# Performance work log

Measured on AMD Instinct MI355X. Metric: run time of the kernel, lower is better.

Reference implementation:

```python
import jax, jax.numpy as jnp
import numpy as np

N_NODES = 100000

def setup_inputs() -> dict:
    key = jax.random.key(0)
    k1, k2, k3, k4, k5, k6 = jax.random.split(key, 6)
    n_edges = 3200000
    edge_rows = jnp.sort(jax.random.randint(k1, (n_edges,), 0, N_NODES))
    edge_cols = jax.random.randint(k2, (n_edges,), 0, N_NODES)
    edge_vals = jax.random.uniform(k3, (n_edges,), dtype=jnp.float32)
    h = jax.random.normal(k4, (N_NODES, 128), dtype=jnp.float32)
    W = jax.random.normal(k5, (128, 128), dtype=jnp.float32) * (1.0 / np.sqrt(128))
    b = jax.random.normal(k6, (128,), dtype=jnp.float32) * 0.01
    return {"edge_rows": edge_rows, "edge_cols": edge_cols, "edge_vals": edge_vals,
            "h": h, "W": W, "b": b}

def reference(edge_rows, edge_cols, edge_vals, h, W, b):
    # SpMM: out[i] = sum over edges e with row[e]==i of vals[e] * h[col[e]]
    msgs = edge_vals[:, None] * h[edge_cols]            # [E, d]
    agg = jax.ops.segment_sum(msgs, edge_rows, num_segments=N_NODES)  # [N, d]
    # Linear + activation (nn.Linear: x @ W.T + b)
    out = agg @ W.T + b
    return jax.nn.relu(out)
```

## Files before the change

kernel.cpp:

```cpp
#include <hip/hip_runtime.h>

#define N_NODES 100000
#define D 128

typedef unsigned short ushort_t;
typedef unsigned char uchar_t;
typedef __attribute__((ext_vector_type(8))) short short8;
typedef __attribute__((ext_vector_type(4))) float f32x4;

__device__ __forceinline__ unsigned f2bf(float x) {
    unsigned u = __float_as_uint(x);
    return (u + 0x7fffu + ((u >> 16) & 1u)) >> 16;
}

__global__ __launch_bounds__(64)
void build_wfrag_kernel(const float* __restrict__ W,
                        ushort_t* __restrict__ Wfrag) {
    const int t  = blockIdx.x;
    const int jt = t >> 2, kt = t & 3;
    const int l  = threadIdx.x;
    const float* src = W + (size_t)(jt * 16 + (l & 15)) * D + kt * 32 + (l >> 4) * 8;
    const float4 p0 = *reinterpret_cast<const float4*>(src);
    const float4 p1 = *reinterpret_cast<const float4*>(src + 4);
    uint4 o;
    o.x = f2bf(p0.x) | (f2bf(p0.y) << 16);
    o.y = f2bf(p0.z) | (f2bf(p0.w) << 16);
    o.z = f2bf(p1.x) | (f2bf(p1.y) << 16);
    o.w = f2bf(p1.z) | (f2bf(p1.w) << 16);
    *reinterpret_cast<uint4*>(Wfrag + ((size_t)t * 64 + l) * 8) = o;
}

__global__ __launch_bounds__(256)
void gemm_Gq_kernel(const float* __restrict__ h,
                    const ushort_t* __restrict__ Wfrag,
                    uchar_t* __restrict__ Gq,
                    float* __restrict__ scales) {
    const int wave = threadIdx.x >> 6;
    const int l    = threadIdx.x & 63;
    const int tile = blockIdx.x * 4 + wave;
    if (tile >= N_NODES / 16) return;
    const int n0   = tile * 16;
    const int lrow = l & 15;
    const int lk   = l >> 4;

    union { short8 v; ushort_t u[8]; } bfrag[4];
    const float* hp = h + (size_t)(n0 + lrow) * D + lk * 8;
#pragma unroll
    for (int kt = 0; kt < 4; ++kt) {
        const float4 q0 = *reinterpret_cast<const float4*>(hp + kt * 32);
        const float4 q1 = *reinterpret_cast<const float4*>(hp + kt * 32 + 4);
        bfrag[kt].u[0] = (ushort_t)f2bf(q0.x);
        bfrag[kt].u[1] = (ushort_t)f2bf(q0.y);
        bfrag[kt].u[2] = (ushort_t)f2bf(q0.z);
        bfrag[kt].u[3] = (ushort_t)f2bf(q0.w);
        bfrag[kt].u[4] = (ushort_t)f2bf(q1.x);
        bfrag[kt].u[5] = (ushort_t)f2bf(q1.y);
        bfrag[kt].u[6] = (ushort_t)f2bf(q1.z);
        bfrag[kt].u[7] = (ushort_t)f2bf(q1.w);
    }

    const uint4* wf = reinterpret_cast<const uint4*>(Wfrag) + l;
    f32x4 acc[8];
#pragma unroll
    for (int jt = 0; jt < 8; ++jt) {
        acc[jt] = (f32x4){0.f, 0.f, 0.f, 0.f};
#pragma unroll
        for (int kt = 0; kt < 4; ++kt) {
            union { uint4 q; short8 v; } af;
            af.q = wf[(jt * 4 + kt) * 64];
            acc[jt] = __builtin_amdgcn_mfma_f32_16x16x32_bf16(
                af.v, bfrag[kt].v, acc[jt], 0, 0, 0);
        }
    }

    float amax = 0.f;
#pragma unroll
    for (int jt = 0; jt < 8; ++jt) {
#pragma unroll
        for (int r = 0; r < 4; ++r) amax = fmaxf(amax, fabsf(acc[jt][r]));
    }
    amax = fmaxf(amax, __shfl_xor(amax, 16));
    amax = fmaxf(amax, __shfl_xor(amax, 32));
    const float s   = amax > 0.f ? amax * (1.f / 127.f) : 1.f;
    const float inv = amax > 0.f ? 127.f / amax : 0.f;

#pragma unroll
    for (int jt = 0; jt < 8; ++jt) {
        const unsigned q0 = (unsigned)((int)rintf(acc[jt][0] * inv) + 128);
        const unsigned q1 = (unsigned)((int)rintf(acc[jt][1] * inv) + 128);
        const unsigned q2 = (unsigned)((int)rintf(acc[jt][2] * inv) + 128);
        const unsigned q3 = (unsigned)((int)rintf(acc[jt][3] * inv) + 128);
        const unsigned pk = q0 | (q1 << 8) | (q2 << 16) | (q3 << 24);
        *reinterpret_cast<unsigned*>(
            Gq + (size_t)(n0 + lrow) * D + jt * 16 + lk * 4) = pk;
    }
    if (l < 16) scales[n0 + l] = s;
}

__global__ __launch_bounds__(256)
void prep_kernel(const int* __restrict__ rows,
                 const int* __restrict__ cols,
                 const float* __restrict__ vals,
                 const float* __restrict__ scales,
                 int* __restrict__ row_ptr,
                 float* __restrict__ vals2, int n_edges) {
    const int e = blockIdx.x * 256 + threadIdx.x;
    if (e >= n_edges) return;

    vals2[e] = vals[e] * scales[cols[e]];

    const int r0 = rows[e];
    if (e == 0) {
        for (int r = 0; r <= r0; ++r) row_ptr[r] = 0;
    }
    if (e + 1 < n_edges) {
        const int r1 = rows[e + 1];
        for (int r = r0 + 1; r <= r1; ++r) row_ptr[r] = e + 1;
    } else {
        for (int r = r0 + 1; r <= N_NODES; ++r) row_ptr[r] = n_edges;
    }
}

__device__ __forceinline__ void accq(float* a, float& vsum, float vs, uint2 g) {
    a[0] += vs * (float)(g.x & 0xffu);
    a[1] += vs * (float)((g.x >> 8) & 0xffu);
    a[2] += vs * (float)((g.x >> 16) & 0xffu);
    a[3] += vs * (float)(g.x >> 24);
    a[4] += vs * (float)(g.y & 0xffu);
    a[5] += vs * (float)((g.y >> 8) & 0xffu);
    a[6] += vs * (float)((g.y >> 16) & 0xffu);
    a[7] += vs * (float)(g.y >> 24);
    vsum += vs;
}

__global__ __launch_bounds__(256)
void gconv_gather_q_kernel(const int* __restrict__ cols,
                           const float* __restrict__ vals2,
                           const uchar_t* __restrict__ Gq,
                           const float* __restrict__ bias,
                           const int* __restrict__ row_ptr,
                           float* __restrict__ out) {
    const int tid  = blockIdx.x * 256 + threadIdx.x;
    const int node = tid >> 4;
    const int il   = tid & 15;
    const unsigned il8 = (unsigned)il * 8u;

    int e = row_ptr[node];
    const int end = row_ptr[node + 1];

    float a[8];
#pragma unroll
    for (int j = 0; j < 8; ++j) a[j] = 0.f;
    float vsum = 0.f;

    for (; e + 7 < end; e += 8) {
        int   c[8];
        float v[8];
        uint2 g[8];
#pragma unroll
        for (int i = 0; i < 8; ++i) c[i] = __builtin_nontemporal_load(cols + e + i);
#pragma unroll
        for (int i = 0; i < 8; ++i) v[i] = __builtin_nontemporal_load(vals2 + e + i);
#pragma unroll
        for (int i = 0; i < 8; ++i)
            g[i] = *reinterpret_cast<const uint2*>(Gq + (((unsigned)c[i] << 7) + il8));
#pragma unroll
        for (int i = 0; i < 8; ++i) accq(a, vsum, v[i], g[i]);
    }
    for (; e < end; ++e) {
        const int   c = __builtin_nontemporal_load(cols + e);
        const float v = __builtin_nontemporal_load(vals2 + e);
        const uint2 g = *reinterpret_cast<const uint2*>(Gq + (((unsigned)c << 7) + il8));
        accq(a, vsum, v, g);
    }

    const float4 b0 = *reinterpret_cast<const float4*>(bias + il8);
    const float4 b1 = *reinterpret_cast<const float4*>(bias + il8 + 4);
    const float corr = 128.f * vsum;
    f32x4 r0, r1;
    r0[0] = a[0] - corr + b0.x; r0[1] = a[1] - corr + b0.y;
    r0[2] = a[2] - corr + b0.z; r0[3] = a[3] - corr + b0.w;
    r1[0] = a[4] - corr + b1.x; r1[1] = a[5] - corr + b1.y;
    r1[2] = a[6] - corr + b1.z; r1[3] = a[7] - corr + b1.w;
#pragma unroll
    for (int i = 0; i < 4; ++i) {
        r0[i] = r0[i] > 0.f ? r0[i] : 0.f;
        r1[i] = r1[i] > 0.f ? r1[i] : 0.f;
    }
    float* op = out + (size_t)node * D + il8;
    __builtin_nontemporal_store(r0, reinterpret_cast<f32x4*>(op));
    __builtin_nontemporal_store(r1, reinterpret_cast<f32x4*>(op + 4));
}

extern "C" void kernel_launch(void* const* d_in, const int* in_sizes, int n_in,
                              void* d_out, int out_size, void* d_ws,
                              size_t ws_size, hipStream_t stream) {
    const int*   edge_rows = (const int*)d_in[0];
    const int*   edge_cols = (const int*)d_in[1];
    const float* edge_vals = (const float*)d_in[2];
    const float* h         = (const float*)d_in[3];
    const float* W         = (const float*)d_in[4];
    const float* b         = (const float*)d_in[5];
    float*       out       = (float*)d_out;

    const int n_edges = in_sizes[0];

    const size_t OFF_RP = 64 * 1024;
    const size_t OFF_SC = OFF_RP + 512 * 1024;
    const size_t OFF_GQ = OFF_SC + 512 * 1024;
    const size_t OFF_V2 = OFF_GQ + (size_t)N_NODES * D;

    ushort_t* Wfrag   = (ushort_t*)d_ws;
    int*      row_ptr = (int*)((char*)d_ws + OFF_RP);
    float*    scales  = (float*)((char*)d_ws + OFF_SC);
    uchar_t*  Gq      = (uchar_t*)((char*)d_ws + OFF_GQ);
    float*    vals2   = (float*)((char*)d_ws + OFF_V2);

    build_wfrag_kernel<<<32, 64, 0, stream>>>(W, Wfrag);

    const int n_tiles     = N_NODES / 16;
    const int gemm_blocks = (n_tiles + 3) / 4;
    gemm_Gq_kernel<<<gemm_blocks, 256, 0, stream>>>(h, Wfrag, Gq, scales);

    prep_kernel<<<(n_edges + 255) / 256, 256, 0, stream>>>(
        edge_rows, edge_cols, edge_vals, scales, row_ptr, vals2, n_edges);

    const int gather_blocks = N_NODES * 16 / 256;
    gconv_gather_q_kernel<<<gather_blocks, 256, 0, stream>>>(
        edge_cols, vals2, Gq, b, row_ptr, out);
}
```

Before: 145.1 us.

## Interleave col/val pairs and gather 16 bytes per lane with 8 lanes per node

The prep kernel now writes column index and scaled value as interleaved int2 pairs, so the gather loads one 8-byte pair per edge instead of two separate streams. The gather kernel drops from 16 to 8 lanes per node, with each lane loading 16 bytes of the quantized row and keeping 16 accumulators. This halves the redundant edge-metadata loads per node and widens each gather load. In exchange it doubles register pressure per thread, halves the thread count, and replaces the nontemporal output stores with plain stores.

New measurement: 129.3 us. 10.9% less time.

```diff
diff --git a/kernel.cpp b/kernel.cpp
--- a/kernel.cpp
+++ b/kernel.cpp
@@ -103,11 +103,12 @@
                  const float* __restrict__ vals,
                  const float* __restrict__ scales,
                  int* __restrict__ row_ptr,
-                 float* __restrict__ vals2, int n_edges) {
+                 int2* __restrict__ pairs, int n_edges) {
     const int e = blockIdx.x * 256 + threadIdx.x;
     if (e >= n_edges) return;
 
-    vals2[e] = vals[e] * scales[cols[e]];
+    const int c = cols[e];
+    pairs[e] = make_int2(c, __float_as_int(vals[e] * scales[c]));
 
     const int r0 = rows[e];
     if (e == 0) {
@@ -121,75 +122,72 @@
     }
 }
 
-__device__ __forceinline__ void accq(float* a, float& vsum, float vs, uint2 g) {
-    a[0] += vs * (float)(g.x & 0xffu);
-    a[1] += vs * (float)((g.x >> 8) & 0xffu);
-    a[2] += vs * (float)((g.x >> 16) & 0xffu);
-    a[3] += vs * (float)(g.x >> 24);
-    a[4] += vs * (float)(g.y & 0xffu);
-    a[5] += vs * (float)((g.y >> 8) & 0xffu);
-    a[6] += vs * (float)((g.y >> 16) & 0xffu);
-    a[7] += vs * (float)(g.y >> 24);
+__device__ __forceinline__ void accq16(float* a, float& vsum, float vs,
+                                       uint4 g) {
+    const unsigned w[4] = {g.x, g.y, g.z, g.w};
+#pragma unroll
+    for (int k = 0; k < 4; ++k) {
+        a[4 * k + 0] += vs * (float)(w[k] & 0xffu);
+        a[4 * k + 1] += vs * (float)((w[k] >> 8) & 0xffu);
+        a[4 * k + 2] += vs * (float)((w[k] >> 16) & 0xffu);
+        a[4 * k + 3] += vs * (float)(w[k] >> 24);
+    }
     vsum += vs;
 }
 
 __global__ __launch_bounds__(256)
-void gconv_gather_q_kernel(const int* __restrict__ cols,
-                           const float* __restrict__ vals2,
-                           const uchar_t* __restrict__ Gq,
-                           const float* __restrict__ bias,
-                           const int* __restrict__ row_ptr,
-                           float* __restrict__ out) {
+void gconv_gather_g8_kernel(const int2* __restrict__ pairs,
+                            const uchar_t* __restrict__ Gq,
+                            const float* __restrict__ bias,
+                            const int* __restrict__ row_ptr,
+                            float* __restrict__ out) {
     const int tid  = blockIdx.x * 256 + threadIdx.x;
-    const int node = tid >> 4;
-    const int il   = tid & 15;
-    const unsigned il8 = (unsigned)il * 8u;
+    const int node = tid >> 3;
+    const int il   = tid & 7;
+    const unsigned il16 = (unsigned)il * 16u;
 
     int e = row_ptr[node];
     const int end = row_ptr[node + 1];
 
-    float a[8];
-#pragma unroll
-    for (int j = 0; j < 8; ++j) a[j] = 0.f;
+    float a[16];
+#pragma unroll
+    for (int j = 0; j < 16; ++j) a[j] = 0.f;
     float vsum = 0.f;
 
     for (; e + 7 < end; e += 8) {
-        int   c[8];
-        float v[8];
-        uint2 g[8];
-#pragma unroll
-        for (int i = 0; i < 8; ++i) c[i] = __builtin_nontemporal_load(cols + e + i);
-#pragma unroll
-        for (int i = 0; i < 8; ++i) v[i] = __builtin_nontemporal_load(vals2 + e + i);
+        int2  p[8];
+        uint4 g[8];
+#pragma unroll
+        for (int i = 0; i < 8; ++i) p[i] = pairs[e + i];
 #pragma unroll
         for (int i = 0; i < 8; ++i)
-            g[i] = *reinterpret_cast<const uint2*>(Gq + (((unsigned)c[i] << 7) + il8));
-#pragma unroll
-        for (int i = 0; i < 8; ++i) accq(a, vsum, v[i], g[i]);
+            g[i] = *reinterpret_cast<const uint4*>(
+                Gq + (((unsigned)p[i].x << 7) + il16));
+#pragma unroll
+        for (int i = 0; i < 8; ++i)
+            accq16(a, vsum, __int_as_float(p[i].y), g[i]);
     }
     for (; e < end; ++e) {
-        const int   c = __builtin_nontemporal_load(cols + e);
-        const float v = __builtin_nontemporal_load(vals2 + e);
-        const uint2 g = *reinterpret_cast<const uint2*>(Gq + (((unsigned)c << 7) + il8));
-        accq(a, vsum, v, g);
-    }
-
-    const float4 b0 = *reinterpret_cast<const float4*>(bias + il8);
-    const float4 b1 = *reinterpret_cast<const float4*>(bias + il8 + 4);
+        const int2 p = pairs[e];
+        const uint4 g = *reinterpret_cast<const uint4*>(
+            Gq + (((unsigned)p.x << 7) + il16));
+        accq16(a, vsum, __int_as_float(p.y), g);
+    }
+
     const float corr = 128.f * vsum;
-    f32x4 r0, r1;
-    r0[0] = a[0] - corr + b0.x; r0[1] = a[1] - corr + b0.y;
-    r0[2] = a[2] - corr + b0.z; r0[3] = a[3] - corr + b0.w;
-    r1[0] = a[4] - corr + b1.x; r1[1] = a[5] - corr + b1.y;
-    r1[2] = a[6] - corr + b1.z; r1[3] = a[7] - corr + b1.w;
-#pragma unroll
-    for (int i = 0; i < 4; ++i) {
-        r0[i] = r0[i] > 0.f ? r0[i] : 0.f;
-        r1[i] = r1[i] > 0.f ? r1[i] : 0.f;
-    }
-    float* op = out + (size_t)node * D + il8;
-    __builtin_nontemporal_store(r0, reinterpret_cast<f32x4*>(op));
-    __builtin_nontemporal_store(r1, reinterpret_cast<f32x4*>(op + 4));
+    float* op = out + (size_t)node * D + il16;
+#pragma unroll
+    for (int q = 0; q < 4; ++q) {
+        const float4 bb = *reinterpret_cast<const float4*>(bias + il16 + q * 4);
+        f32x4 r;
+        r[0] = a[4 * q + 0] - corr + bb.x;
+        r[1] = a[4 * q + 1] - corr + bb.y;
+        r[2] = a[4 * q + 2] - corr + bb.z;
+        r[3] = a[4 * q + 3] - corr + bb.w;
+#pragma unroll
+        for (int i = 0; i < 4; ++i) r[i] = r[i] > 0.f ? r[i] : 0.f;
+        *reinterpret_cast<f32x4*>(op + q * 4) = r;
+    }
 }
 
 extern "C" void kernel_launch(void* const* d_in, const int* in_sizes, int n_in,
@@ -208,13 +206,13 @@
     const size_t OFF_RP = 64 * 1024;
     const size_t OFF_SC = OFF_RP + 512 * 1024;
     const size_t OFF_GQ = OFF_SC + 512 * 1024;
-    const size_t OFF_V2 = OFF_GQ + (size_t)N_NODES * D;
+    const size_t OFF_PR = OFF_GQ + (size_t)N_NODES * D;
 
     ushort_t* Wfrag   = (ushort_t*)d_ws;
     int*      row_ptr = (int*)((char*)d_ws + OFF_RP);
     float*    scales  = (float*)((char*)d_ws + OFF_SC);
     uchar_t*  Gq      = (uchar_t*)((char*)d_ws + OFF_GQ);
-    float*    vals2   = (float*)((char*)d_ws + OFF_V2);
+    int2*     pairs   = (int2*)((char*)d_ws + OFF_PR);
 
     build_wfrag_kernel<<<32, 64, 0, stream>>>(W, Wfrag);
 
@@ -223,9 +221,9 @@
     gemm_Gq_kernel<<<gemm_blocks, 256, 0, stream>>>(h, Wfrag, Gq, scales);
 
     prep_kernel<<<(n_edges + 255) / 256, 256, 0, stream>>>(
-        edge_rows, edge_cols, edge_vals, scales, row_ptr, vals2, n_edges);
-
-    const int gather_blocks = N_NODES * 16 / 256;
-    gconv_gather_q_kernel<<<gather_blocks, 256, 0, stream>>>(
-        edge_cols, vals2, Gq, b, row_ptr, out);
-}
+        edge_rows, edge_cols, edge_vals, scales, row_ptr, pairs, n_edges);
+
+    const int gather_blocks = N_NODES * 8 / 256;
+    gconv_gather_g8_kernel<<<gather_blocks, 256, 0, stream>>>(
+        pairs, Gq, b, row_ptr, out);
+}
```
